# Kernel optimization log

Hardware: AMD Instinct MI355X
Metric: run time of the kernel (lower is better)

## Reference

```python
import jax, jax.numpy as jnp
import numpy as np

DIM = 128
HEADS = 4
WIN = 7
N = WIN * WIN  # 49 tokens per window
B = 64         # images
BDIM = 64      # windows per image (56/7)^2
B_ = B * BDIM  # 4096 total windows
HEAD_DIM = DIM // HEADS
SCALE = HEAD_DIM ** (-0.5)


def _rel_index():
    ch, cw = np.meshgrid(np.arange(WIN), np.arange(WIN), indexing='ij')
    coords = np.stack([ch.ravel(), cw.ravel()])            # [2, N]
    rel = coords[:, :, None] - coords[:, None, :]          # [2, N, N]
    rel = rel.transpose(1, 2, 0).astype(np.int32)
    rel[:, :, 0] += WIN - 1
    rel[:, :, 1] += WIN - 1
    rel[:, :, 0] *= 2 * WIN - 1
    return jnp.asarray(rel.sum(-1))                        # [N, N] in [0, 169)


def setup_inputs() -> dict:
    key = jax.random.key(0)
    ks = jax.random.split(key, 7)
    return {
        'x': jax.random.normal(ks[0], (B_, N, DIM), jnp.float32),
        'q_global': jax.random.normal(ks[1], (B, 1, HEADS, N, HEAD_DIM), jnp.float32),
        'rel_bias_table': jax.random.normal(ks[2], (169, HEADS), jnp.float32) * 0.02,
        'W_kv': jax.random.normal(ks[3], (DIM, 2 * DIM), jnp.float32) / np.sqrt(DIM),
        'b_kv': jnp.zeros((2 * DIM,), jnp.float32),
        'W_proj': jax.random.normal(ks[4], (DIM, DIM), jnp.float32) / np.sqrt(DIM),
        'b_proj': jnp.zeros((DIM,), jnp.float32),
        'rel_index': _rel_index(),
    }


def reference(x, q_global, rel_bias_table, W_kv, b_kv, W_proj, b_proj, rel_index):
    Bw, n, C = x.shape
    Bg = q_global.shape[0]
    bdim = Bw // Bg
    # kv projection: [B_, N, 2, H, hd] -> k, v each [B_, H, N, hd]
    kv = (x @ W_kv + b_kv).reshape(Bw, n, 2, HEADS, HEAD_DIM)
    kv = kv.transpose(2, 0, 3, 1, 4)
    k, v = kv[0], kv[1]
    # broadcast global q over windows of each image
    q = jnp.broadcast_to(q_global, (Bg, bdim, HEADS, n, HEAD_DIM)).reshape(Bw, HEADS, n, HEAD_DIM)
    attn = jnp.einsum('bhnd,bhmd->bhnm', q * SCALE, k)
    bias = rel_bias_table[rel_index]                        # [N, N, H]
    attn = attn + bias.transpose(2, 0, 1)[None]
    attn = jax.nn.softmax(attn, axis=-1)
    out = jnp.einsum('bhnm,bhmd->bhnd', attn, v)
    out = out.transpose(0, 2, 1, 3).reshape(Bw, n, C)
    return out @ W_proj + b_proj
```

## Files before the change

### kernel.cpp

```cpp
#include <hip/hip_runtime.h>

#define SCALE 0.17677669529663687f

typedef __attribute__((ext_vector_type(8))) short bf16x8;
typedef __attribute__((ext_vector_type(4))) float f32x4;

__device__ inline short cvt_bf16(float f) {
    union { float f; unsigned u; } v; v.f = f;
    unsigned r = v.u + 0x7fffu + ((v.u >> 16) & 1u);
    return (short)(r >> 16);
}

#define WS_WPT  32768
#define WS_QW   49152
#define WS_BIAS 450560

__global__ void prep_kernel(const float* __restrict__ qg,
                            const float* __restrict__ rbt,
                            const float* __restrict__ wkv,
                            const float* __restrict__ wpj,
                            const int*   __restrict__ ridx,
                            short* __restrict__ ws) {
    int i = blockIdx.x * 256 + threadIdx.x;
    if (i < 32768) {
        int c = i >> 7, k = i & 127;
        ws[i] = cvt_bf16(wkv[k * 256 + c]);
        return;
    }
    i -= 32768;
    if (i < 16384) {
        int c = i >> 7, k = i & 127;
        ws[WS_WPT + i] = cvt_bf16(wpj[k * 128 + c]);
        return;
    }
    i -= 16384;
    if (i < 100352) {
        float4 q4 = *(const float4*)(qg + (long)i * 4);
        short p0 = cvt_bf16(q4.x * SCALE), p1 = cvt_bf16(q4.y * SCALE);
        short p2 = cvt_bf16(q4.z * SCALE), p3 = cvt_bf16(q4.w * SCALE);
        unsigned lo = (unsigned short)p0 | ((unsigned)(unsigned short)p1 << 16);
        unsigned hi = (unsigned short)p2 | ((unsigned)(unsigned short)p3 << 16);
        uint2 u; u.x = lo; u.y = hi;
        *(uint2*)(ws + WS_QW + (long)i * 4) = u;
        return;
    }
    i -= 100352;
    if (i < 12544) {
        int h = i / 3136, rem = i % 3136, ir = rem >> 6, j = rem & 63;
        float* bias = (float*)(ws + WS_BIAS);
        bias[i] = (j < 49) ? rbt[ridx[ir * 49 + j] * 4 + h] : 0.f;
    }
}

#define SLOT    3744
#define VTS_OFF 15840
#define SMEM_SZ 25056

__global__ __launch_bounds__(256, 3) void win_attn_kernel(
        const float* __restrict__ x,
        const short* __restrict__ ws,
        const float* __restrict__ bkv,
        const float* __restrict__ bpj,
        float* __restrict__ out) {
    const int b    = blockIdx.x;
    const int img  = b >> 6;
    const int tid  = threadIdx.x;
    const int w    = tid >> 6;
    const int lane = tid & 63;
    const int quad = lane >> 4;
    const int l16  = lane & 15;

    const short* wkvt  = ws;
    const short* wpt   = ws + WS_WPT;
    const short* qw    = ws + WS_QW;
    const float* biasb = (const float*)(ws + WS_BIAS);

    __shared__ __align__(16) short smem[SMEM_SZ];
    short* regA = smem;
    short* vts  = smem + VTS_OFF;
    short* os   = smem;

    const f32x4 fzero = {0.f, 0.f, 0.f, 0.f};
    const int h = w;

    bf16x8 afrag[4][4];
    const float* xb = x + (long)b * 49 * 128;
    #pragma unroll
    for (int mi = 0; mi < 4; ++mi) {
        int tok = mi * 16 + l16; if (tok > 48) tok = 48;
        #pragma unroll
        for (int kk = 0; kk < 4; ++kk) {
            const float* xr = xb + tok * 128 + kk * 32 + quad * 8;
            float4 a = *(const float4*)xr;
            float4 c = *(const float4*)(xr + 4);
            bf16x8 f;
            f[0] = cvt_bf16(a.x); f[1] = cvt_bf16(a.y);
            f[2] = cvt_bf16(a.z); f[3] = cvt_bf16(a.w);
            f[4] = cvt_bf16(c.x); f[5] = cvt_bf16(c.y);
            f[6] = cvt_bf16(c.z); f[7] = cvt_bf16(c.w);
            afrag[mi][kk] = f;
        }
    }
    const short* qh = qw + (long)(img * 4 + h) * 49 * 32;
    bf16x8 qfrag[4];
    #pragma unroll
    for (int ni = 0; ni < 4; ++ni) {
        int i = ni * 16 + l16; if (i > 48) i = 48;
        qfrag[ni] = *(const bf16x8*)(qh + i * 32 + quad * 8);
    }

    #pragma unroll
    for (int nt = 0; nt < 4; ++nt) {
        const int c0 = (w * 4 + nt) * 16;
        f32x4 acc[4] = {fzero, fzero, fzero, fzero};
        #pragma unroll
        for (int kk = 0; kk < 4; ++kk) {
            bf16x8 bfrag = *(const bf16x8*)(wkvt + (c0 + l16) * 128 + kk * 32 + quad * 8);
            #pragma unroll
            for (int mi = 0; mi < 4; ++mi)
                acc[mi] = __builtin_amdgcn_mfma_f32_16x16x32_bf16(afrag[mi][kk], bfrag, acc[mi], 0, 0, 0);
        }
        const int c = c0 + l16;
        const float bias = bkv[c];
        #pragma unroll
        for (int mi = 0; mi < 4; ++mi)
            #pragma unroll
            for (int r = 0; r < 4; ++r) {
                int tok = mi * 16 + quad * 4 + r;
                short val = cvt_bf16(acc[mi][r] + bias);
                if (c < 128) {
                    int hh = c >> 5, d = c & 31;
                    regA[hh * SLOT + tok * 40 + d] = val;
                } else {
                    int cv = c - 128, hh = cv >> 5, d = cv & 31;
                    vts[(hh * 32 + d) * 72 + tok] = val;
                }
            }
    }
    __syncthreads();

    short* ksh = regA + h * SLOT;
    bf16x8 kfrag[4];
    #pragma unroll
    for (int mi = 0; mi < 4; ++mi)
        kfrag[mi] = *(const bf16x8*)(ksh + (mi * 16 + l16) * 40 + quad * 8);

    f32x4 sacc[4][4];
    #pragma unroll
    for (int mi = 0; mi < 4; ++mi)
        #pragma unroll
        for (int ni = 0; ni < 4; ++ni) sacc[mi][ni] = fzero;
    #pragma unroll
    for (int ni = 0; ni < 4; ++ni)
        #pragma unroll
        for (int mi = 0; mi < 4; ++mi)
            sacc[mi][ni] = __builtin_amdgcn_mfma_f32_16x16x32_bf16(kfrag[mi], qfrag[ni], sacc[mi][ni], 0, 0, 0);

    #pragma unroll
    for (int ni = 0; ni < 4; ++ni) {
        int itok = ni * 16 + l16;
        int ic = itok > 48 ? 48 : itok;
        const float* bp = biasb + (h * 49 + ic) * 64;
        float v[16];
        #pragma unroll
        for (int mi = 0; mi < 4; ++mi) {
            float4 b4 = *(const float4*)(bp + mi * 16 + quad * 4);
            float bb[4] = {b4.x, b4.y, b4.z, b4.w};
            #pragma unroll
            for (int r = 0; r < 4; ++r) {
                int j = mi * 16 + quad * 4 + r;
                v[mi * 4 + r] = (j < 49) ? (sacc[mi][ni][r] + bb[r]) : -3.0e38f;
            }
        }
        float m = v[0];
        #pragma unroll
        for (int t = 1; t < 16; ++t) m = fmaxf(m, v[t]);
        m = fmaxf(m, __shfl_xor(m, 16, 64));
        m = fmaxf(m, __shfl_xor(m, 32, 64));
        float sum = 0.f;
        #pragma unroll
        for (int t = 0; t < 16; ++t) { float e = __expf(v[t] - m); v[t] = e; sum += e; }
        sum += __shfl_xor(sum, 16, 64);
        sum += __shfl_xor(sum, 32, 64);
        float inv = 1.0f / sum;
        if (itok < 52) {
            #pragma unroll
            for (int mi = 0; mi < 4; ++mi) {
                short p0 = cvt_bf16(v[mi * 4 + 0] * inv), p1 = cvt_bf16(v[mi * 4 + 1] * inv);
                short p2 = cvt_bf16(v[mi * 4 + 2] * inv), p3 = cvt_bf16(v[mi * 4 + 3] * inv);
                unsigned lo = (unsigned short)p0 | ((unsigned)(unsigned short)p1 << 16);
                unsigned hi = (unsigned short)p2 | ((unsigned)(unsigned short)p3 << 16);
                uint2 u; u.x = lo; u.y = hi;
                *(uint2*)(ksh + itok * 72 + mi * 16 + quad * 4) = u;
            }
        }
    }

    f32x4 oacc[4][2];
    #pragma unroll
    for (int mo = 0; mo < 4; ++mo)
        #pragma unroll
        for (int nt = 0; nt < 2; ++nt) oacc[mo][nt] = fzero;
    #pragma unroll
    for (int kk = 0; kk < 2; ++kk) {
        bf16x8 pfrag[4];
        #pragma unroll
        for (int mo = 0; mo < 4; ++mo)
            pfrag[mo] = *(const bf16x8*)(ksh + (mo * 16 + l16) * 72 + kk * 32 + quad * 8);
        #pragma unroll
        for (int nt = 0; nt < 2; ++nt) {
            bf16x8 vfrag = *(const bf16x8*)(vts + (h * 32 + nt * 16 + l16) * 72 + kk * 32 + quad * 8);
            #pragma unroll
            for (int mo = 0; mo < 4; ++mo)
                oacc[mo][nt] = __builtin_amdgcn_mfma_f32_16x16x32_bf16(pfrag[mo], vfrag, oacc[mo][nt], 0, 0, 0);
        }
    }
    __syncthreads();

    #pragma unroll
    for (int mo = 0; mo < 4; ++mo)
        #pragma unroll
        for (int nt = 0; nt < 2; ++nt)
            #pragma unroll
            for (int r = 0; r < 4; ++r) {
                int tok = mo * 16 + quad * 4 + r;
                os[tok * 136 + h * 32 + nt * 16 + l16] = cvt_bf16(oacc[mo][nt][r]);
            }
    __syncthreads();

    bf16x8 ofrag[4][4];
    #pragma unroll
    for (int mi = 0; mi < 4; ++mi)
        #pragma unroll
        for (int kk = 0; kk < 4; ++kk)
            ofrag[mi][kk] = *(const bf16x8*)(os + (mi * 16 + l16) * 136 + kk * 32 + quad * 8);
    #pragma unroll
    for (int ct = 0; ct < 2; ++ct) {
        const int c0 = (w * 2 + ct) * 16;
        f32x4 pacc[4] = {fzero, fzero, fzero, fzero};
        #pragma unroll
        for (int kk = 0; kk < 4; ++kk) {
            bf16x8 wfrag = *(const bf16x8*)(wpt + (c0 + l16) * 128 + kk * 32 + quad * 8);
            #pragma unroll
            for (int mi = 0; mi < 4; ++mi)
                pacc[mi] = __builtin_amdgcn_mfma_f32_16x16x32_bf16(ofrag[mi][kk], wfrag, pacc[mi], 0, 0, 0);
        }
        const float bb = bpj[c0 + l16];
        #pragma unroll
        for (int mi = 0; mi < 4; ++mi)
            #pragma unroll
            for (int r = 0; r < 4; ++r) {
                int tok = mi * 16 + quad * 4 + r;
                if (tok < 49)
                    out[((long)b * 49 + tok) * 128 + c0 + l16] = pacc[mi][r] + bb;
            }
    }
}

extern "C" void kernel_launch(void* const* d_in, const int* in_sizes, int n_in,
                              void* d_out, int out_size, void* d_ws, size_t ws_size,
                              hipStream_t stream) {
    const float* x    = (const float*)d_in[0];
    const float* qg   = (const float*)d_in[1];
    const float* rbt  = (const float*)d_in[2];
    const float* wkv  = (const float*)d_in[3];
    const float* bkv  = (const float*)d_in[4];
    const float* wpj  = (const float*)d_in[5];
    const float* bpj  = (const float*)d_in[6];
    const int*   ridx = (const int*)d_in[7];
    short* ws = (short*)d_ws;

    const int prep_total = 32768 + 16384 + 100352 + 12544;
    prep_kernel<<<(prep_total + 255) / 256, 256, 0, stream>>>(qg, rbt, wkv, wpj, ridx, ws);
    win_attn_kernel<<<4096, 256, 0, stream>>>(x, ws, bkv, bpj, (float*)d_out);
}
```

Measured before the change: 309.8 us.

## Shrink LDS layout with XOR-swizzled P and packed bf16 conversion for 4 blocks/CU

Compacts the shared-memory layout: P rows use a 64-element stride with an XOR swizzle, V^T rows use stride 56, and a zeroed tail covers reads past the end. This cuts LDS per block and raises launch bounds to 4 blocks per CU, aiming for higher occupancy. It also replaces round-to-nearest-even bf16 conversion with cheaper round-half-up packing using v_perm, which shifts rounding slightly. Row clamping and the tail handling must stay correct, because the padded region is no longer written by the V stores.

```diff
diff --git a/kernel.cpp b/kernel.cpp
--- a/kernel.cpp
+++ b/kernel.cpp
@@ -9,6 +9,14 @@
     union { float f; unsigned u; } v; v.f = f;
     unsigned r = v.u + 0x7fffu + ((v.u >> 16) & 1u);
     return (short)(r >> 16);
+}
+__device__ inline short cvt_bf16_fast(float f) {
+    union { float f; unsigned u; } v; v.f = f;
+    return (short)((v.u + 0x8000u) >> 16);
+}
+__device__ inline unsigned pack_bf16x2(float f0, float f1) {
+    union { float f; unsigned u; } a, b; a.f = f0; b.f = f1;
+    return __builtin_amdgcn_perm(b.u + 0x8000u, a.u + 0x8000u, 0x07060302u);
 }
 
 #define WS_WPT  32768
@@ -36,10 +44,10 @@
     i -= 16384;
     if (i < 100352) {
         float4 q4 = *(const float4*)(qg + (long)i * 4);
-        short p0 = cvt_bf16(q4.x * SCALE), p1 = cvt_bf16(q4.y * SCALE);
-        short p2 = cvt_bf16(q4.z * SCALE), p3 = cvt_bf16(q4.w * SCALE);
-        unsigned lo = (unsigned short)p0 | ((unsigned)(unsigned short)p1 << 16);
-        unsigned hi = (unsigned short)p2 | ((unsigned)(unsigned short)p3 << 16);
+        unsigned lo = (unsigned)(unsigned short)cvt_bf16(q4.x * SCALE) |
+                      ((unsigned)(unsigned short)cvt_bf16(q4.y * SCALE) << 16);
+        unsigned hi = (unsigned)(unsigned short)cvt_bf16(q4.z * SCALE) |
+                      ((unsigned)(unsigned short)cvt_bf16(q4.w * SCALE) << 16);
         uint2 u; u.x = lo; u.y = hi;
         *(uint2*)(ws + WS_QW + (long)i * 4) = u;
         return;
@@ -52,11 +60,12 @@
     }
 }
 
-#define SLOT    3744
-#define VTS_OFF 15840
-#define SMEM_SZ 25056
-
-__global__ __launch_bounds__(256, 3) void win_attn_kernel(
+#define PSLOT   3136
+#define VOFF    12544
+#define VSTR    56
+#define SMEM_SZ 19776
+
+__global__ __launch_bounds__(256, 4) void win_attn_kernel(
         const float* __restrict__ x,
         const short* __restrict__ ws,
         const float* __restrict__ bkv,
@@ -76,9 +85,9 @@
     const float* biasb = (const float*)(ws + WS_BIAS);
 
     __shared__ __align__(16) short smem[SMEM_SZ];
-    short* regA = smem;
-    short* vts  = smem + VTS_OFF;
-    short* os   = smem;
+    short* os = smem;
+
+    if (tid < 64) smem[19712 + tid] = 0;
 
     const f32x4 fzero = {0.f, 0.f, 0.f, 0.f};
     const int h = w;
@@ -93,12 +102,12 @@
             const float* xr = xb + tok * 128 + kk * 32 + quad * 8;
             float4 a = *(const float4*)xr;
             float4 c = *(const float4*)(xr + 4);
-            bf16x8 f;
-            f[0] = cvt_bf16(a.x); f[1] = cvt_bf16(a.y);
-            f[2] = cvt_bf16(a.z); f[3] = cvt_bf16(a.w);
-            f[4] = cvt_bf16(c.x); f[5] = cvt_bf16(c.y);
-            f[6] = cvt_bf16(c.z); f[7] = cvt_bf16(c.w);
-            afrag[mi][kk] = f;
+            union { uint4 u; bf16x8 v; } pk;
+            pk.u.x = pack_bf16x2(a.x, a.y);
+            pk.u.y = pack_bf16x2(a.z, a.w);
+            pk.u.z = pack_bf16x2(c.x, c.y);
+            pk.u.w = pack_bf16x2(c.z, c.w);
+            afrag[mi][kk] = pk.v;
         }
     }
     const short* qh = qw + (long)(img * 4 + h) * 49 * 32;
@@ -121,25 +130,33 @@
                 acc[mi] = __builtin_amdgcn_mfma_f32_16x16x32_bf16(afrag[mi][kk], bfrag, acc[mi], 0, 0, 0);
         }
         const int c = c0 + l16;
-        const float bias = bkv[c];
-        #pragma unroll
-        for (int mi = 0; mi < 4; ++mi)
-            #pragma unroll
-            for (int r = 0; r < 4; ++r) {
-                int tok = mi * 16 + quad * 4 + r;
-                short val = cvt_bf16(acc[mi][r] + bias);
-                if (c < 128) {
-                    int hh = c >> 5, d = c & 31;
-                    regA[hh * SLOT + tok * 40 + d] = val;
-                } else {
-                    int cv = c - 128, hh = cv >> 5, d = cv & 31;
-                    vts[(hh * 32 + d) * 72 + tok] = val;
+        const float bv = bkv[c];
+        if (c < 128) {
+            int hh = c >> 5, d = c & 31;
+            short* kdst = smem + hh * PSLOT + d;
+            #pragma unroll
+            for (int mi = 0; mi < 4; ++mi)
+                #pragma unroll
+                for (int r = 0; r < 4; ++r) {
+                    int tok = mi * 16 + quad * 4 + r;
+                    kdst[tok * 40] = cvt_bf16_fast(acc[mi][r] + bv);
                 }
-            }
+        } else {
+            int cv = c - 128, hh = cv >> 5, d = cv & 31;
+            short* vdst = smem + VOFF + (hh * 32 + d) * VSTR;
+            #pragma unroll
+            for (int mi = 0; mi < 4; ++mi) {
+                int tok0 = mi * 16 + quad * 4;
+                if (tok0 < VSTR) {
+                    *(unsigned*)(vdst + tok0)     = pack_bf16x2(acc[mi][0] + bv, acc[mi][1] + bv);
+                    *(unsigned*)(vdst + tok0 + 2) = pack_bf16x2(acc[mi][2] + bv, acc[mi][3] + bv);
+                }
+            }
+        }
     }
     __syncthreads();
 
-    short* ksh = regA + h * SLOT;
+    short* ksh = smem + h * PSLOT;
     bf16x8 kfrag[4];
     #pragma unroll
     for (int mi = 0; mi < 4; ++mi)
@@ -183,15 +200,15 @@
         sum += __shfl_xor(sum, 16, 64);
         sum += __shfl_xor(sum, 32, 64);
         float inv = 1.0f / sum;
-        if (itok < 52) {
+        if (itok < 49) {
             #pragma unroll
             for (int mi = 0; mi < 4; ++mi) {
-                short p0 = cvt_bf16(v[mi * 4 + 0] * inv), p1 = cvt_bf16(v[mi * 4 + 1] * inv);
-                short p2 = cvt_bf16(v[mi * 4 + 2] * inv), p3 = cvt_bf16(v[mi * 4 + 3] * inv);
-                unsigned lo = (unsigned short)p0 | ((unsigned)(unsigned short)p1 << 16);
-                unsigned hi = (unsigned short)p2 | ((unsigned)(unsigned short)p3 << 16);
-                uint2 u; u.x = lo; u.y = hi;
-                *(uint2*)(ksh + itok * 72 + mi * 16 + quad * 4) = u;
+                int jo8 = mi * 2 + (quad >> 1);
+                int off = itok * 64 + ((jo8 ^ (itok & 7)) << 3) + ((quad & 1) << 2);
+                uint2 u;
+                u.x = pack_bf16x2(v[mi * 4 + 0] * inv, v[mi * 4 + 1] * inv);
+                u.y = pack_bf16x2(v[mi * 4 + 2] * inv, v[mi * 4 + 3] * inv);
+                *(uint2*)(ksh + off) = u;
             }
         }
     }
@@ -205,11 +222,14 @@
     for (int kk = 0; kk < 2; ++kk) {
         bf16x8 pfrag[4];
         #pragma unroll
-        for (int mo = 0; mo < 4; ++mo)
-            pfrag[mo] = *(const bf16x8*)(ksh + (mo * 16 + l16) * 72 + kk * 32 + quad * 8);
+        for (int mo = 0; mo < 4; ++mo) {
+            int row = mo * 16 + l16; if (row > 48) row = 48;
+            int jo8 = kk * 4 + quad;
+            pfrag[mo] = *(const bf16x8*)(ksh + row * 64 + ((jo8 ^ (row & 7)) << 3));
+        }
         #pragma unroll
         for (int nt = 0; nt < 2; ++nt) {
-            bf16x8 vfrag = *(const bf16x8*)(vts + (h * 32 + nt * 16 + l16) * 72 + kk * 32 + quad * 8);
+            bf16x8 vfrag = *(const bf16x8*)(smem + VOFF + (h * 32 + nt * 16 + l16) * VSTR + kk * 32 + quad * 8);
             #pragma unroll
             for (int mo = 0; mo < 4; ++mo)
                 oacc[mo][nt] = __builtin_amdgcn_mfma_f32_16x16x32_bf16(pfrag[mo], vfrag, oacc[mo][nt], 0, 0, 0);
@@ -224,7 +244,7 @@
             #pragma unroll
             for (int r = 0; r < 4; ++r) {
                 int tok = mo * 16 + quad * 4 + r;
-                os[tok * 136 + h * 32 + nt * 16 + l16] = cvt_bf16(oacc[mo][nt][r]);
+                os[tok * 136 + h * 32 + nt * 16 + l16] = cvt_bf16_fast(oacc[mo][nt][r]);
             }
     __syncthreads();
 
```

New measurement: 300.1 us. 3.1% less time.
